# Optimization experiments

Hardware: AMD Instinct MI355X
Metric: run time of the kernel (lower is better)

The kernel has to match this reference:

```python
import jax, jax.numpy as jnp
import numpy as np

N = 4096
INPUT_DIM = 256
HIDDEN = 64
HEADS = 8
NEG_SLOPE = 0.2
MASK_FILL = -10000.0


def setup_inputs() -> dict:
    key = jax.random.key(0)
    k_x, k_adj, k_w, k_as, k_ad = jax.random.split(key, 5)
    x = jax.random.normal(k_x, (N, INPUT_DIM), dtype=jnp.float32)
    adjacency = jax.random.bernoulli(k_adj, 0.05, (N, N)) | jnp.eye(N, dtype=bool)
    # linear weight, torch convention: [out_features, in_features]
    W = jax.random.normal(k_w, (HEADS * HIDDEN, INPUT_DIM), dtype=jnp.float32) * 0.05
    attn_src = jax.random.normal(k_as, (HEADS, HIDDEN), dtype=jnp.float32) * 0.1
    attn_dst = jax.random.normal(k_ad, (HEADS, HIDDEN), dtype=jnp.float32) * 0.1
    return {"x": x, "adjacency": adjacency, "W": W, "attn_src": attn_src, "attn_dst": attn_dst}


def reference(x, adjacency, W, attn_src, attn_dst):
    # h: [N, heads, hidden]
    h = (x @ W.T).reshape(N, HEADS, HIDDEN)
    src_scores = jnp.einsum('nhd,hd->nh', h, attn_src)  # [N, heads]
    dst_scores = jnp.einsum('nhd,hd->nh', h, attn_dst)  # [N, heads]
    # logits[i, j, h] = src[i, h] + dst[j, h]  (matches torch permute(2,0,1) layout math)
    logits = src_scores[:, None, :] + dst_scores[None, :, :]  # [N, N, heads]
    logits = jax.nn.leaky_relu(logits, negative_slope=NEG_SLOPE)
    logits = jnp.where(adjacency[:, :, None], logits, MASK_FILL)
    alpha = jax.nn.softmax(logits, axis=1)  # softmax over source nodes j
    out = jnp.einsum('ijh,jhf->ihf', alpha, h)  # [N, heads, hidden]
    return out.mean(axis=1)  # [N, hidden]
```

## Files before the change

### kernel.cpp

```cpp
#include <hip/hip_runtime.h>

#define NN 4096
#define IN_DIM 256
#define HID 64
#define HEADS 8

typedef __attribute__((ext_vector_type(4))) float f32x4;
typedef __attribute__((ext_vector_type(8))) short s16x8;
typedef unsigned short u16;
typedef unsigned long long u64;

__device__ inline u16 f2bf(float f) {
  union { float f; unsigned u; } v; v.f = f;
  unsigned r = (v.u + 0x7FFFu + ((v.u >> 16) & 1u)) >> 16;
  return (u16)r;
}
__device__ inline float bf2f(u16 b) {
  union { unsigned u; float f; } v; v.u = ((unsigned)b) << 16;
  return v.f;
}
__device__ __forceinline__ unsigned cvt_pk_bf16(float a, float b) {
  unsigned r;
  asm("v_cvt_pk_bf16_f32 %0, %1, %2" : "=v"(r) : "v"(a), "v"(b));
  return r;
}
__device__ inline unsigned encf(float f) {
  unsigned u = __float_as_uint(f);
  return (u & 0x80000000u) ? ~u : (u | 0x80000000u);
}
__device__ inline float decf(unsigned k) {
  return (k & 0x80000000u) ? __uint_as_float(k & 0x7FFFFFFFu) : __uint_as_float(~k);
}

__global__ __launch_bounds__(256) void gat_main(
    const void* __restrict__ adj, const float* __restrict__ x,
    const float* __restrict__ W, const float* __restrict__ a_src,
    const float* __restrict__ a_dst, u16* __restrict__ Hbt,
    float* __restrict__ s_srcT, float* __restrict__ s_dstT,
    unsigned* __restrict__ Mh_enc, u64* __restrict__ bits)
{
  __shared__ u16 xhi[64 * 72], xlo[64 * 72], whi[64 * 72], wlo[64 * 72];
  __shared__ int smode;
  const int t = threadIdx.x;
  const int bid = blockIdx.x;

  if (bid >= 512) {
    if (t < 64) {
      const unsigned char* a8 = (const unsigned char*)adj;
      const int* a32 = (const int*)adj;
      size_t i8 = (size_t)(4 * t + 1) * 4097;
      int p8 = a8[i8] != 0;
      size_t k = (size_t)(2 * t + 1);
      int p32 = a32[k * 4097] != 0;
      int p64 = a32[2 * k * 4097] != 0;
      int ok8 = __all(p8), ok32 = __all(p32), ok64 = __all(p64);
      if (t == 0) smode = ok8 ? 0 : (ok32 ? 1 : (ok64 ? 2 : 1));
    }
    __syncthreads();
    const int mode = smode;
    const int lane = t & 63;
    const int wave = (bid - 512) * 4 + (t >> 6);
    const int nwaves = 1536 * 4;
    const size_t nwords = (size_t)NN * NN / 64;
    for (size_t w = wave; w < nwords; w += nwaves) {
      size_t e = w * 64 + lane;
      int on;
      if (mode == 1)      on = ((const int*)adj)[e] != 0;
      else if (mode == 0) on = ((const unsigned char*)adj)[e] != 0;
      else                on = ((const long long*)adj)[e] != 0;
      u64 b = __ballot(on);
      if (lane == 0) bits[w] = b;
    }
    return;
  }

  const int nb = bid & 63;
  const int ob = bid >> 6;
  const int lane = t & 63, wid = t >> 6;
  const int wr = wid >> 1, wc = wid & 1;
  const int g = lane >> 4;

  f32x4 acc[2][2] = {};

  const int sn = t >> 2;
  const int skc = (t & 3) * 16;

  for (int kb = 0; kb < 4; ++kb) {
    const float* xr = x + (size_t)(nb * 64 + sn) * IN_DIM + kb * 64 + skc;
    const float* wr_p = W + (size_t)(ob * 64 + sn) * IN_DIM + kb * 64 + skc;
#pragma unroll
    for (int c = 0; c < 4; ++c) {
      float4 xv = ((const float4*)xr)[c];
      float4 wv = ((const float4*)wr_p)[c];
      float xf[4] = {xv.x, xv.y, xv.z, xv.w};
      float wf[4] = {wv.x, wv.y, wv.z, wv.w};
      u16 xh[4], xl[4], wh[4], wl[4];
#pragma unroll
      for (int e = 0; e < 4; ++e) {
        xh[e] = f2bf(xf[e]); xl[e] = f2bf(xf[e] - bf2f(xh[e]));
        wh[e] = f2bf(wf[e]); wl[e] = f2bf(wf[e] - bf2f(wh[e]));
      }
      int base = sn * 72 + skc + c * 4;
      *(ushort4*)(xhi + base) = make_ushort4(xh[0], xh[1], xh[2], xh[3]);
      *(ushort4*)(xlo + base) = make_ushort4(xl[0], xl[1], xl[2], xl[3]);
      *(ushort4*)(whi + base) = make_ushort4(wh[0], wh[1], wh[2], wh[3]);
      *(ushort4*)(wlo + base) = make_ushort4(wl[0], wl[1], wl[2], wl[3]);
    }
    __syncthreads();
#pragma unroll
    for (int ks = 0; ks < 2; ++ks) {
      const int k0 = ks * 32 + g * 8;
      s16x8 ah[2], al[2], bh[2], bl[2];
#pragma unroll
      for (int nf = 0; nf < 2; ++nf) {
        int row = wr * 32 + nf * 16 + (lane & 15);
        ah[nf] = *(const s16x8*)(xhi + row * 72 + k0);
        al[nf] = *(const s16x8*)(xlo + row * 72 + k0);
      }
#pragma unroll
      for (int of = 0; of < 2; ++of) {
        int row = wc * 32 + of * 16 + (lane & 15);
        bh[of] = *(const s16x8*)(whi + row * 72 + k0);
        bl[of] = *(const s16x8*)(wlo + row * 72 + k0);
      }
#pragma unroll
      for (int nf = 0; nf < 2; ++nf)
#pragma unroll
        for (int of = 0; of < 2; ++of) {
          acc[nf][of] = __builtin_amdgcn_mfma_f32_16x16x32_bf16(ah[nf], bh[of], acc[nf][of], 0, 0, 0);
          acc[nf][of] = __builtin_amdgcn_mfma_f32_16x16x32_bf16(ah[nf], bl[of], acc[nf][of], 0, 0, 0);
          acc[nf][of] = __builtin_amdgcn_mfma_f32_16x16x32_bf16(al[nf], bh[of], acc[nf][of], 0, 0, 0);
        }
    }
    __syncthreads();
  }

  u16* Ct = xhi;
#pragma unroll
  for (int nf = 0; nf < 2; ++nf)
#pragma unroll
    for (int of = 0; of < 2; ++of)
#pragma unroll
      for (int r = 0; r < 4; ++r) {
        int nloc = wr * 32 + nf * 16 + g * 4 + r;
        int oloc = wc * 32 + of * 16 + (lane & 15);
        Ct[oloc * 72 + nloc] = f2bf(acc[nf][of][r]);
      }

  {
    const float* asp = a_src + ob * 64;
    const float* adp = a_dst + ob * 64;
    float as0 = asp[wc * 32 + (lane & 15)], as1 = asp[wc * 32 + 16 + (lane & 15)];
    float ad0 = adp[wc * 32 + (lane & 15)], ad1 = adp[wc * 32 + 16 + (lane & 15)];
    float* sred = (float*)wlo;
#pragma unroll
    for (int nf = 0; nf < 2; ++nf)
#pragma unroll
      for (int r = 0; r < 4; ++r) {
        float vs = acc[nf][0][r] * as0 + acc[nf][1][r] * as1;
        float vd = acc[nf][0][r] * ad0 + acc[nf][1][r] * ad1;
#pragma unroll
        for (int m = 1; m < 16; m <<= 1) { vs += __shfl_xor(vs, m); vd += __shfl_xor(vd, m); }
        if ((lane & 15) == 0) {
          int node = wr * 32 + nf * 16 + g * 4 + r;
          sred[wc * 64 + node] = vs;
          sred[128 + wc * 64 + node] = vd;
        }
      }
  }
  __syncthreads();
  {
    int o = t >> 2, nc = (t & 3) * 16;
    u16* dst = Hbt + ((size_t)(ob * 64 + nb) * 64 + o) * 64 + nc;
#pragma unroll
    for (int c = 0; c < 2; ++c) {
      s16x8 v = *(const s16x8*)(Ct + o * 72 + nc + c * 8);
      *(s16x8*)(dst + c * 8) = v;
    }
  }
  if (t < 64) {
    const float* sred = (const float*)wlo;
    float vssum = sred[t] + sred[64 + t];
    float vdsum = sred[128 + t] + sred[192 + t];
    s_srcT[(size_t)ob * NN + nb * 64 + t] = vssum;
    s_dstT[(size_t)ob * NN + nb * 64 + t] = vdsum;
    float m = vdsum;
#pragma unroll
    for (int s = 1; s < 64; s <<= 1) m = fmaxf(m, __shfl_xor(m, s));
    if (t == 0) atomicMax(Mh_enc + ob, encf(m));
  }
}

__global__ __launch_bounds__(512, 4) void gat_flash(
    const u64* __restrict__ bits, const u16* __restrict__ Hbt,
    const float* __restrict__ s_srcT, const float* __restrict__ s_dstT,
    const unsigned* __restrict__ Mh_enc, float* __restrict__ pout)
{
  __shared__ char shmem[32768];
  __shared__ float Lbuf[8][16];
  u16* Ast = (u16*)shmem;

  const int t = threadIdx.x, lane = t & 63, wid = t >> 6;
  const int ws4 = wid & 3, jh = wid >> 2;
  const int bid = blockIdx.x;
  const int h = bid & 7, iblk = bid >> 3;
  const int i_loc = lane & 15, g = lane >> 4, j0 = g * 8;
  const int irow = iblk * 64 + ws4 * 16 + i_loc;

  const float s_i = s_srcT[(size_t)h * NN + irow];
  float m_i = s_i + decf(Mh_enc[h]);
  m_i = fmaxf(m_i, 0.2f * m_i);
  const float L2E = 1.44269504f;
  const float mL = m_i * L2E;

  const u16* tile0 = Hbt + (size_t)h * 64 * 4096;
  const float* dT = s_dstT + (size_t)h * NN;

  const int lt = t & 255;
  const int r0 = lt >> 3, colE = (lt & 7) * 8;
  const int jtb = jh * 32;
  const u16* gsrc0 = tile0 + (size_t)jtb * 4096 + r0 * 64 + (colE ^ ((r0 & 7) << 3));
  const u16* gsrc1 = tile0 + (size_t)jtb * 4096 + (32 + r0) * 64 + (colE ^ ((r0 & 7) << 3));
  const u64* brow = bits + (size_t)irow * 64 + jtb;
  const float* dp = dT + jtb * 64 + j0;

  u16* sdstA = Ast + jh * 8192;
  u16* sdstB = sdstA + 4096;
  const char* lbaseA = (const char*)sdstA;
  const char* lbaseB = (const char*)sdstB;
  const int swz = (i_loc & 7) << 4;
  const int ofA0 = (g * 16) ^ swz, ofA1 = ((g * 16) + 64) ^ swz;

  s16x8 ones;
#pragma unroll
  for (int e = 0; e < 8; ++e) ones[e] = (short)0x3F80;

  f32x4 acc[4] = {};
  f32x4 acc_l = {0.f, 0.f, 0.f, 0.f};

#define QUAD(DV, MBITS, SH, PW0, PW1) do {                            \
    float z0 = s_i + DV[0], z1 = s_i + DV[1];                         \
    float z2 = s_i + DV[2], z3 = s_i + DV[3];                         \
    z0 = fmaxf(z0, 0.2f * z0); z1 = fmaxf(z1, 0.2f * z1);             \
    z2 = fmaxf(z2, 0.2f * z2); z3 = fmaxf(z3, 0.2f * z3);             \
    float e0 = __builtin_amdgcn_exp2f(__builtin_fmaf(z0, L2E, -mL));  \
    float e1 = __builtin_amdgcn_exp2f(__builtin_fmaf(z1, L2E, -mL));  \
    float e2 = __builtin_amdgcn_exp2f(__builtin_fmaf(z2, L2E, -mL));  \
    float e3 = __builtin_amdgcn_exp2f(__builtin_fmaf(z3, L2E, -mL));  \
    e0 = ((MBITS >> (SH + 0)) & 1u) ? e0 : 0.f;                       \
    e1 = ((MBITS >> (SH + 1)) & 1u) ? e1 : 0.f;                       \
    e2 = ((MBITS >> (SH + 2)) & 1u) ? e2 : 0.f;                       \
    e3 = ((MBITS >> (SH + 3)) & 1u) ? e3 : 0.f;                       \
    PW0 = cvt_pk_bf16(e0, e1); PW1 = cvt_pk_bf16(e2, e3);             \
  } while (0)

#define TILE_BODY(SDST, LBASE) do {                                   \
    *(s16x8*)((SDST) + lt * 8) = sv0;                                 \
    *(s16x8*)((SDST) + 2048 + lt * 8) = sv1;                          \
    gsrc0 += 4096; gsrc1 += 4096;                                     \
    sv0 = *(const s16x8*)(gsrc0);                                     \
    sv1 = *(const s16x8*)(gsrc1);                                     \
    const u64 am_ = *brow++;                                          \
    f32x4 d0 = *(const f32x4*)(dp);                                   \
    f32x4 d1 = *(const f32x4*)(dp + 4);                               \
    f32x4 d2 = *(const f32x4*)(dp + 32);                              \
    f32x4 d3 = *(const f32x4*)(dp + 36);                              \
    dp += 64;                                                         \
    const unsigned amlo = (unsigned)(am_ >> j0);                      \
    const unsigned amhi = (unsigned)(am_ >> (32 + j0));               \
    union { unsigned w_[4]; s16x8 v_; } P0, P1;                       \
    QUAD(d0, amlo, 0, P0.w_[0], P0.w_[1]);                            \
    QUAD(d1, amlo, 4, P0.w_[2], P0.w_[3]);                            \
    QUAD(d2, amhi, 0, P1.w_[0], P1.w_[1]);                            \
    QUAD(d3, amhi, 4, P1.w_[2], P1.w_[3]);                            \
    __syncthreads();                                                  \
    _Pragma("unroll")                                                 \
    for (int fb = 0; fb < 4; ++fb) {                                  \
      const int rowb = (fb * 16 + i_loc) * 128;                       \
      s16x8 A0 = *(const s16x8*)((LBASE) + rowb + ofA0);              \
      s16x8 A1 = *(const s16x8*)((LBASE) + rowb + ofA1);              \
      acc[fb] = __builtin_amdgcn_mfma_f32_16x16x32_bf16(A0, P0.v_, acc[fb], 0, 0, 0); \
      acc[fb] = __builtin_amdgcn_mfma_f32_16x16x32_bf16(A1, P1.v_, acc[fb], 0, 0, 0); \
    }                                                                 \
    acc_l = __builtin_amdgcn_mfma_f32_16x16x32_bf16(ones, P0.v_, acc_l, 0, 0, 0); \
    acc_l = __builtin_amdgcn_mfma_f32_16x16x32_bf16(ones, P1.v_, acc_l, 0, 0, 0); \
  } while (0)

  s16x8 sv0 = *(const s16x8*)(gsrc0);
  s16x8 sv1 = *(const s16x8*)(gsrc1);

  for (int it = 0; it < 16; ++it) {
    TILE_BODY(sdstA, lbaseA);
    TILE_BODY(sdstB, lbaseB);
  }
#undef QUAD
#undef TILE_BODY

  float l_run = acc_l[0];
  if (lane < 16) Lbuf[wid][i_loc] = l_run;

  __syncthreads();
  float* accst = (float*)shmem;
  if (jh == 1) {
    float* ab = accst + (ws4 * 16 + i_loc) * 66;
#pragma unroll
    for (int fb = 0; fb < 4; ++fb)
      *(f32x4*)(ab + fb * 16 + g * 4) = acc[fb];
  }
  __syncthreads();
  if (jh == 0) {
    const float invL = 1.f / (l_run + Lbuf[4 + ws4][i_loc]);
    float* ob = pout + ((size_t)h * NN + irow) * 64;
#pragma unroll
    for (int fb = 0; fb < 4; ++fb) {
      f32x4 v = acc[fb] +
          *(const f32x4*)(accst + (ws4 * 16 + i_loc) * 66 + fb * 16 + g * 4);
      *(f32x4*)(ob + fb * 16 + g * 4) = v * invL;
    }
  }
}

__global__ __launch_bounds__(256) void gat_combine(
    const float* __restrict__ pout, float* __restrict__ out)
{
  size_t e = (size_t)blockIdx.x * 256 + threadIdx.x;
  f32x4 s = {0.f, 0.f, 0.f, 0.f};
#pragma unroll
  for (int h = 0; h < 8; ++h)
    s += ((const f32x4*)pout)[(size_t)h * (NN * 16) + e];
  ((f32x4*)out)[e] = s * 0.125f;
}

extern "C" void kernel_launch(void* const* d_in, const int* in_sizes, int n_in,
                              void* d_out, int out_size, void* d_ws, size_t ws_size,
                              hipStream_t stream)
{
  const float* x = (const float*)d_in[0];
  const void* adj = d_in[1];
  const float* W = (const float*)d_in[2];
  const float* a_src = (const float*)d_in[3];
  const float* a_dst = (const float*)d_in[4];
  float* out = (float*)d_out;

  char* ws = (char*)d_ws;
  float* pout = (float*)ws;
  u16* Hbt = (u16*)(ws + 8 * 1024 * 1024);
  float* s_srcT = (float*)(ws + 12 * 1024 * 1024);
  float* s_dstT = (float*)(ws + 12 * 1024 * 1024 + 128 * 1024);
  unsigned* Mh_enc = (unsigned*)(ws + 12 * 1024 * 1024 + 384 * 1024);
  u64* bits = (u64*)(ws + 12 * 1024 * 1024 + 512 * 1024);

  hipMemsetAsync(Mh_enc, 0, 32, stream);
  gat_main<<<2048, 256, 0, stream>>>(adj, x, W, a_src, a_dst, Hbt,
                                     s_srcT, s_dstT, Mh_enc, bits);
  gat_flash<<<512, 512, 0, stream>>>(bits, Hbt, s_srcT, s_dstT, Mh_enc, pout);
  gat_combine<<<256, 256, 0, stream>>>(pout, out);
}
```

Baseline: 106.2 us.

## Split fused adjacency-pack and projection GEMM kernel into two launches

The kernel that used one grid for both the adjacency bit-packing (blocks 512 and up) and the x@W^T projection (blocks below 512) is split into two separate kernels launched back to back on the same stream. The packing kernel now uses 2048 blocks, all for packing, so the grid-stride loop is spread over more waves. The GEMM uses a 2D grid of 64x8 blocks. The change removes the heterogeneous-block scheduling, at the cost of an extra launch and serialising the two phases, which previously could overlap.

```diff
diff --git a/kernel.cpp b/kernel.cpp
--- a/kernel.cpp
+++ b/kernel.cpp
@@ -32,50 +32,51 @@
   return (k & 0x80000000u) ? __uint_as_float(k & 0x7FFFFFFFu) : __uint_as_float(~k);
 }
 
-__global__ __launch_bounds__(256) void gat_main(
-    const void* __restrict__ adj, const float* __restrict__ x,
-    const float* __restrict__ W, const float* __restrict__ a_src,
-    const float* __restrict__ a_dst, u16* __restrict__ Hbt,
-    float* __restrict__ s_srcT, float* __restrict__ s_dstT,
-    unsigned* __restrict__ Mh_enc, u64* __restrict__ bits)
-{
-  __shared__ u16 xhi[64 * 72], xlo[64 * 72], whi[64 * 72], wlo[64 * 72];
+__global__ __launch_bounds__(256) void gat_pack(
+    const void* __restrict__ adj, u64* __restrict__ bits)
+{
   __shared__ int smode;
   const int t = threadIdx.x;
-  const int bid = blockIdx.x;
-
-  if (bid >= 512) {
-    if (t < 64) {
-      const unsigned char* a8 = (const unsigned char*)adj;
-      const int* a32 = (const int*)adj;
-      size_t i8 = (size_t)(4 * t + 1) * 4097;
-      int p8 = a8[i8] != 0;
-      size_t k = (size_t)(2 * t + 1);
-      int p32 = a32[k * 4097] != 0;
-      int p64 = a32[2 * k * 4097] != 0;
-      int ok8 = __all(p8), ok32 = __all(p32), ok64 = __all(p64);
-      if (t == 0) smode = ok8 ? 0 : (ok32 ? 1 : (ok64 ? 2 : 1));
-    }
-    __syncthreads();
-    const int mode = smode;
-    const int lane = t & 63;
-    const int wave = (bid - 512) * 4 + (t >> 6);
-    const int nwaves = 1536 * 4;
-    const size_t nwords = (size_t)NN * NN / 64;
-    for (size_t w = wave; w < nwords; w += nwaves) {
-      size_t e = w * 64 + lane;
-      int on;
-      if (mode == 1)      on = ((const int*)adj)[e] != 0;
-      else if (mode == 0) on = ((const unsigned char*)adj)[e] != 0;
-      else                on = ((const long long*)adj)[e] != 0;
-      u64 b = __ballot(on);
-      if (lane == 0) bits[w] = b;
-    }
-    return;
-  }
-
-  const int nb = bid & 63;
-  const int ob = bid >> 6;
+  if (t < 64) {
+    const unsigned char* a8 = (const unsigned char*)adj;
+    const int* a32 = (const int*)adj;
+    size_t i8 = (size_t)(4 * t + 1) * 4097;
+    int p8 = a8[i8] != 0;
+    size_t k = (size_t)(2 * t + 1);
+    int p32 = a32[k * 4097] != 0;
+    int p64 = a32[2 * k * 4097] != 0;
+    int ok8 = __all(p8), ok32 = __all(p32), ok64 = __all(p64);
+    if (t == 0) smode = ok8 ? 0 : (ok32 ? 1 : (ok64 ? 2 : 1));
+  }
+  __syncthreads();
+  const int mode = smode;
+
+  const int lane = t & 63;
+  const int wave = (blockIdx.x * blockDim.x + t) >> 6;
+  const int nwaves = (gridDim.x * blockDim.x) >> 6;
+  const size_t nwords = (size_t)NN * NN / 64;
+
+  for (size_t w = wave; w < nwords; w += nwaves) {
+    size_t e = w * 64 + lane;
+    int on;
+    if (mode == 1)      on = ((const int*)adj)[e] != 0;
+    else if (mode == 0) on = ((const unsigned char*)adj)[e] != 0;
+    else                on = ((const long long*)adj)[e] != 0;
+    u64 b = __ballot(on);
+    if (lane == 0) bits[w] = b;
+  }
+}
+
+__global__ __launch_bounds__(256) void gat_gemm1(
+    const float* __restrict__ x, const float* __restrict__ W,
+    const float* __restrict__ a_src, const float* __restrict__ a_dst,
+    u16* __restrict__ Hbt, float* __restrict__ s_srcT,
+    float* __restrict__ s_dstT, unsigned* __restrict__ Mh_enc)
+{
+  __shared__ u16 xhi[64 * 72], xlo[64 * 72], whi[64 * 72], wlo[64 * 72];
+  const int nb = blockIdx.x;
+  const int ob = blockIdx.y;
+  const int t = threadIdx.x;
   const int lane = t & 63, wid = t >> 6;
   const int wr = wid >> 1, wc = wid & 1;
   const int g = lane >> 4;
@@ -351,8 +352,9 @@
   u64* bits = (u64*)(ws + 12 * 1024 * 1024 + 512 * 1024);
 
   hipMemsetAsync(Mh_enc, 0, 32, stream);
-  gat_main<<<2048, 256, 0, stream>>>(adj, x, W, a_src, a_dst, Hbt,
-                                     s_srcT, s_dstT, Mh_enc, bits);
+  gat_pack<<<2048, 256, 0, stream>>>(adj, bits);
+  gat_gemm1<<<dim3(64, 8), 256, 0, stream>>>(x, W, a_src, a_dst, Hbt,
+                                             s_srcT, s_dstT, Mh_enc);
   gat_flash<<<512, 512, 0, stream>>>(bits, Hbt, s_srcT, s_dstT, Mh_enc, pout);
   gat_combine<<<256, 256, 0, stream>>>(pout, out);
 }
```

New measurement: 98.50 us. 7.2% less time.
